# Kernel tuning notes

Measured on AMD Instinct MI355X. Metric: run time of the kernel, lower is better.

## Reference

```python
import jax, jax.numpy as jnp
import numpy as np

NUM_CAMS = 1
NUM_HEADS = 1
NUM_LEVELS = 1
NUM_POINTS = 4
NUM_DEPTH = 128
EMBED = 128  # must equal NUM_DEPTH (output_proj is applied to the depth axis)


def setup_inputs() -> dict:
    key0 = jax.random.key(0)
    ks = jax.random.split(key0, 12)
    bsv, nq, nv = 1, 1024, 1024  # nq == nv == H*W (32*32)
    off_dim = NUM_CAMS * NUM_HEADS * NUM_LEVELS * NUM_DEPTH * NUM_POINTS * 2  # 1024
    aw_dim = NUM_CAMS * NUM_HEADS * NUM_LEVELS * NUM_DEPTH * NUM_POINTS       # 512
    return {
        "query": jax.random.normal(ks[0], (bsv, nq, EMBED), jnp.float32),
        "key": jax.random.normal(ks[1], (NUM_CAMS, nv, bsv, EMBED), jnp.float32),
        "value": jax.random.normal(ks[2], (NUM_CAMS, nv, bsv, EMBED), jnp.float32),
        "ref_3d": jax.random.uniform(ks[3], (bsv * NUM_CAMS, nq * NUM_DEPTH, 2), jnp.float32),
        "spatial_shapes": jnp.array([[32, 32]], dtype=jnp.int32),
        "W_off": jax.random.normal(ks[4], (EMBED, off_dim), jnp.float32) * 0.02,
        "b_off": jax.random.normal(ks[5], (off_dim,), jnp.float32) * 0.02,
        "W_attn": jax.random.normal(ks[6], (EMBED, aw_dim), jnp.float32) * 0.02,
        "b_attn": jax.random.normal(ks[7], (aw_dim,), jnp.float32) * 0.02,
        "W_v": jax.random.normal(ks[8], (EMBED, EMBED), jnp.float32) / np.sqrt(EMBED),
        "b_v": jnp.zeros((EMBED,), jnp.float32),
        "W_o": jax.random.normal(ks[9], (EMBED, EMBED), jnp.float32) / np.sqrt(EMBED),
        "b_o": jnp.zeros((EMBED,), jnp.float32),
    }


def _bilinear_sample(val, H, W, x, y):
    """grid_sample(align_corners=False, padding=zeros) equivalent.
    val: [B, H*W, D]; x, y: [B, Q, P] in pixel coords. Returns [B, Q, P, D]."""
    B, Q, P = x.shape
    D = val.shape[-1]
    x0f = jnp.floor(x); y0f = jnp.floor(y)
    ix0 = x0f.astype(jnp.int32); iy0 = y0f.astype(jnp.int32)
    wx1 = x - x0f; wy1 = y - y0f
    wx0 = 1.0 - wx1; wy0 = 1.0 - wy1

    def corner(ix, iy, w):
        valid = (ix >= 0) & (ix < W) & (iy >= 0) & (iy < H)
        idx = jnp.clip(iy, 0, H - 1) * W + jnp.clip(ix, 0, W - 1)  # [B,Q,P]
        g = jnp.take_along_axis(val, idx.reshape(B, Q * P)[:, :, None], axis=1)
        g = g.reshape(B, Q, P, D)
        return g * (w * valid.astype(val.dtype))[..., None]

    return (corner(ix0, iy0, wx0 * wy0)
            + corner(ix0 + 1, iy0, wx1 * wy0)
            + corner(ix0, iy0 + 1, wx0 * wy1)
            + corner(ix0 + 1, iy0 + 1, wx1 * wy1))


def reference(query, key, value, ref_3d, spatial_shapes,
              W_off, b_off, W_attn, b_attn, W_v, b_v, W_o, b_o):
    bsv, nq, E = query.shape
    cams, nv, bs, _ = key.shape
    identity = query

    # key/value: [cams, nv, bs, E] -> [bsv, nv, E]
    key2 = jnp.transpose(key, (2, 0, 1, 3)).reshape(bsv, nv, E)
    val = jnp.flip(value, axis=0)
    val = jnp.transpose(val, (2, 0, 1, 3)).reshape(bsv, nv, E)
    val = val @ W_v + b_v
    val = val.reshape(bsv * cams, nv, E)  # num_heads=1 -> head_dim=E

    # offsets / attention weights (heads=levels=1 axes squeezed)
    off = (query @ W_off + b_off).reshape(bsv, nq, cams, NUM_DEPTH, NUM_POINTS, 2)
    aw = (query @ W_attn + b_attn).reshape(bsv, nq, cams, NUM_DEPTH, NUM_LEVELS * NUM_POINTS)
    aw = jax.nn.softmax(aw, axis=-1).reshape(bsv, nq, cams, NUM_DEPTH, NUM_POINTS)
    off = jnp.transpose(off, (0, 2, 1, 3, 4, 5)).reshape(bsv * cams, nq * NUM_DEPTH, NUM_POINTS, 2)
    aw = jnp.transpose(aw, (0, 2, 1, 3, 4)).reshape(bsv * cams, nq * NUM_DEPTH, NUM_POINTS)

    H = spatial_shapes[0, 0]
    W = spatial_shapes[0, 1]
    norm = jnp.stack([W, H]).astype(off.dtype)  # [W, H]
    loc = ref_3d[:, :, None, :] + off / norm    # [B, Qe, P, 2] in [0,1]
    x = loc[..., 0] * W.astype(loc.dtype) - 0.5
    y = loc[..., 1] * H.astype(loc.dtype) - 0.5

    sampled = _bilinear_sample(val, H, W, x, y)          # [B, Qe, P, E]
    out = jnp.einsum('bqpe,bqp->bqe', sampled, aw)       # weighted sum over points

    out = out.reshape(bsv, cams, nq, NUM_DEPTH, E).mean(axis=1)  # [bsv, nq, depth, E]
    out = (out * key2[:, :, None, :]).mean(axis=-1)              # [bsv, nq, depth]
    out = out @ W_o + b_o                                        # depth == EMBED
    return out + identity  # dropout = identity in eval
```

## Files before the change

kernel.cpp:

```cpp
#include <hip/hip_runtime.h>
#include <hip/hip_bf16.h>


#define NQ   1024
#define NV   1024
#define ND   128
#define NP   4
#define IMG_W 32
#define IMG_H 32

__device__ __forceinline__ void gemm_tile64(
    const float* __restrict__ A,
    const float* __restrict__ B,
    int N, bool nt,
    const float* __restrict__ bias,
    const float* __restrict__ cvec,
    float* __restrict__ C,
    int m0, int n0, float* sA, float* sB) {
  const int tid = threadIdx.x;

#pragma unroll
  for (int k = 0; k < 8; ++k) {
    int c = tid + k * 256;
    int m = c & 63, e4 = c >> 6;
    const float4 v = *(const float4*)(A + (size_t)(m0 + m) * 128 + e4 * 4);
    sA[(e4 * 4 + 0) * 64 + m] = v.x;
    sA[(e4 * 4 + 1) * 64 + m] = v.y;
    sA[(e4 * 4 + 2) * 64 + m] = v.z;
    sA[(e4 * 4 + 3) * 64 + m] = v.w;
  }
  if (nt) {
#pragma unroll
    for (int k = 0; k < 8; ++k) {
      int c = tid + k * 256;
      int n = c & 63, e4 = c >> 6;
      const float4 v = *(const float4*)(B + (size_t)(n0 + n) * 128 + e4 * 4);
      sB[(e4 * 4 + 0) * 64 + n] = v.x;
      sB[(e4 * 4 + 1) * 64 + n] = v.y;
      sB[(e4 * 4 + 2) * 64 + n] = v.z;
      sB[(e4 * 4 + 3) * 64 + n] = v.w;
    }
  } else {
#pragma unroll
    for (int k = 0; k < 8; ++k) {
      int c = tid + k * 256;
      int n4 = c & 15, e = c >> 4;
      *(float4*)(sB + e * 64 + n4 * 4) =
          *(const float4*)(B + (size_t)e * N + n0 + n4 * 4);
    }
  }
  __syncthreads();

  const int tx = tid & 15, ty = tid >> 4;
  float acc[4][4] = {};
#pragma unroll 8
  for (int e = 0; e < 128; ++e) {
    const float4 a = *(const float4*)(sA + e * 64 + ty * 4);
    const float4 b = *(const float4*)(sB + e * 64 + tx * 4);
    acc[0][0] += a.x * b.x; acc[0][1] += a.x * b.y; acc[0][2] += a.x * b.z; acc[0][3] += a.x * b.w;
    acc[1][0] += a.y * b.x; acc[1][1] += a.y * b.y; acc[1][2] += a.y * b.z; acc[1][3] += a.y * b.w;
    acc[2][0] += a.z * b.x; acc[2][1] += a.z * b.y; acc[2][2] += a.z * b.z; acc[2][3] += a.z * b.w;
    acc[3][0] += a.w * b.x; acc[3][1] += a.w * b.y; acc[3][2] += a.w * b.z; acc[3][3] += a.w * b.w;
  }

  float4 bv = make_float4(0.f, 0.f, 0.f, 0.f);
  if (bias) bv = *(const float4*)(bias + n0 + tx * 4);
#pragma unroll
  for (int i = 0; i < 4; ++i) {
    const int m = m0 + ty * 4 + i;
    float cv = cvec ? cvec[m] : 0.f;
    float4 r;
    r.x = acc[i][0] + bv.x + cv;
    r.y = acc[i][1] + bv.y + cv;
    r.z = acc[i][2] + bv.z + cv;
    r.w = acc[i][3] + bv.w + cv;
    *(float4*)(C + (size_t)m * N + n0 + tx * 4) = r;
  }
}

__global__ __launch_bounds__(256, 2) void p1_kernel(
    const float* __restrict__ query, const float* __restrict__ key,
    const float* __restrict__ W_off, const float* __restrict__ b_off,
    const float* __restrict__ W_attn, const float* __restrict__ b_attn,
    const float* __restrict__ W_v, const float* __restrict__ b_v,
    float* __restrict__ off_ws, float* __restrict__ aw_ws,
    float* __restrict__ keyp_ws, float* __restrict__ c_ws) {
  __shared__ float sA[128 * 64];
  __shared__ float sB[128 * 64];
  const int t = blockIdx.x;
  if (t < 256) {
    gemm_tile64(query, W_off, 1024, false, b_off, nullptr, off_ws,
                (t >> 4) * 64, (t & 15) * 64, sA, sB);
  } else if (t < 384) {
    const int u = t - 256;
    gemm_tile64(query, W_attn, 512, false, b_attn, nullptr, aw_ws,
                (u >> 3) * 64, (u & 7) * 64, sA, sB);
  } else if (t < 416) {
    const int u = t - 384;
    gemm_tile64(key, W_v, 128, true, nullptr, nullptr, keyp_ws,
                (u >> 1) * 64, (u & 1) * 64, sA, sB);
  } else {
    for (int i = 0; i < 4; ++i) {
      const int q = threadIdx.x + i * 256;
      float s = 0.f;
      for (int e = 0; e < 128; ++e) s += key[(size_t)q * 128 + e] * b_v[e];
      c_ws[q] = s;
    }
  }
}

__global__ __launch_bounds__(256, 2) void p2_kernel(
    const float* __restrict__ keyp_ws, const float* __restrict__ value,
    const float* __restrict__ c_ws, float* __restrict__ dotv_ws) {
  __shared__ float sA[128 * 64];
  __shared__ float sB[128 * 64];
  const int t = blockIdx.x;
  gemm_tile64(keyp_ws, value, 1024, true, nullptr, c_ws, dotv_ws,
              (t >> 4) * 64, (t & 15) * 64, sA, sB);
}

__global__ __launch_bounds__(256) void p3_kernel(
    const float* __restrict__ dotv,
    const float* __restrict__ off,
    const float* __restrict__ awr,
    const float* __restrict__ ref3d,
    const float* __restrict__ query,
    const float* __restrict__ W_o,
    const float* __restrict__ b_o,
    float* __restrict__ out) {
  __shared__ float img[2][NV];
  __shared__ float o1s[2][ND];

  const int tid = threadIdx.x;
  const int q0 = blockIdx.x * 2;

#pragma unroll
  for (int k = 0; k < 2; ++k) {
    int c = tid + k * 256;
    int qq = c >> 8, v4 = c & 255;
    *(float4*)(&img[qq][v4 * 4]) =
        *(const float4*)(dotv + (size_t)(q0 + qq) * NV + v4 * 4);
  }
  __syncthreads();

  {
    const int qq = tid >> 7;
    const int q = q0 + qq;
    const int d = tid & 127;
    const float* im = img[qq];
    const size_t qe = (size_t)q * ND + d;

    const float rx = ref3d[qe * 2 + 0];
    const float ry = ref3d[qe * 2 + 1];

    const float* awp = awr + (size_t)q * (ND * NP) + d * NP;
    const float a0 = awp[0], a1 = awp[1], a2 = awp[2], a3 = awp[3];
    const float mx = fmaxf(fmaxf(a0, a1), fmaxf(a2, a3));
    const float e0 = __expf(a0 - mx), e1 = __expf(a1 - mx),
                e2 = __expf(a2 - mx), e3 = __expf(a3 - mx);
    const float inv = 1.0f / (e0 + e1 + e2 + e3);
    const float w[4] = {e0 * inv, e1 * inv, e2 * inv, e3 * inv};

    const float* op = off + (size_t)q * (ND * NP * 2) + d * (NP * 2);

    float acc = 0.0f;
#pragma unroll
    for (int p = 0; p < NP; ++p) {
      const float x = rx * (float)IMG_W + op[p * 2 + 0] - 0.5f;
      const float y = ry * (float)IMG_H + op[p * 2 + 1] - 0.5f;
      const float xf = floorf(x), yf = floorf(y);
      const int ix0 = (int)xf, iy0 = (int)yf;
      const float wx1 = x - xf, wy1 = y - yf;
      const float wx0 = 1.0f - wx1, wy0 = 1.0f - wy1;

      float s = 0.0f;
#pragma unroll
      for (int cy = 0; cy < 2; ++cy) {
#pragma unroll
        for (int cx = 0; cx < 2; ++cx) {
          const int ix = ix0 + cx, iy = iy0 + cy;
          const bool valid = (ix >= 0) & (ix < IMG_W) & (iy >= 0) & (iy < IMG_H);
          const int cix = min(max(ix, 0), IMG_W - 1);
          const int ciy = min(max(iy, 0), IMG_H - 1);
          const float wgt = (cx ? wx1 : wx0) * (cy ? wy1 : wy0);
          s += valid ? im[ciy * IMG_W + cix] * wgt : 0.0f;
        }
      }
      acc += w[p] * s;
    }
    o1s[qq][d] = acc * (1.0f / 128.0f);
  }
  __syncthreads();

  {
    const int qq = tid >> 7;
    const int q = q0 + qq;
    const int n = tid & 127;
    float acc = b_o[n] + query[(size_t)q * 128 + n];
#pragma unroll 8
    for (int d = 0; d < 128; ++d)
      acc += o1s[qq][d] * W_o[(size_t)d * 128 + n];
    out[(size_t)q * 128 + n] = acc;
  }
}

extern "C" void kernel_launch(void* const* d_in, const int* in_sizes, int n_in,
                              void* d_out, int out_size, void* d_ws, size_t ws_size,
                              hipStream_t stream) {
  const float* query  = (const float*)d_in[0];
  const float* key    = (const float*)d_in[1];
  const float* value  = (const float*)d_in[2];
  const float* ref3d  = (const float*)d_in[3];
  const float* W_off  = (const float*)d_in[5];
  const float* b_off  = (const float*)d_in[6];
  const float* W_attn = (const float*)d_in[7];
  const float* b_attn = (const float*)d_in[8];
  const float* W_v    = (const float*)d_in[9];
  const float* b_v    = (const float*)d_in[10];
  const float* W_o    = (const float*)d_in[11];
  const float* b_o    = (const float*)d_in[12];
  float* out = (float*)d_out;

  float* ws = (float*)d_ws;
  float* off_ws  = ws;
  float* aw_ws   = off_ws + (size_t)NQ * 1024;
  float* keyp_ws = aw_ws + (size_t)NQ * 512;
  float* c_ws    = keyp_ws + (size_t)NQ * 128;
  float* dotv_ws = c_ws + 1024;

  p1_kernel<<<417, 256, 0, stream>>>(query, key, W_off, b_off, W_attn, b_attn,
                                     W_v, b_v, off_ws, aw_ws, keyp_ws, c_ws);
  p2_kernel<<<256, 256, 0, stream>>>(keyp_ws, value, c_ws, dotv_ws);
  p3_kernel<<<512, 256, 0, stream>>>(dotv_ws, off_ws, aw_ws, ref3d, query,
                                     W_o, b_o, out);
}
```

Baseline: 113.7 us.

## Fuse three kernels into one monolithic per-query-block kernel with bf16 MFMA

```diff
diff --git a/kernel.cpp b/kernel.cpp
--- a/kernel.cpp
+++ b/kernel.cpp
@@ -1,5 +1,4 @@
 #include <hip/hip_runtime.h>
-#include <hip/hip_bf16.h>
 
 
 #define NQ   1024
@@ -8,143 +7,189 @@
 #define NP   4
 #define IMG_W 32
 #define IMG_H 32
-
-__device__ __forceinline__ void gemm_tile64(
-    const float* __restrict__ A,
-    const float* __restrict__ B,
-    int N, bool nt,
-    const float* __restrict__ bias,
-    const float* __restrict__ cvec,
-    float* __restrict__ C,
-    int m0, int n0, float* sA, float* sB) {
-  const int tid = threadIdx.x;
-
-#pragma unroll
-  for (int k = 0; k < 8; ++k) {
-    int c = tid + k * 256;
-    int m = c & 63, e4 = c >> 6;
-    const float4 v = *(const float4*)(A + (size_t)(m0 + m) * 128 + e4 * 4);
-    sA[(e4 * 4 + 0) * 64 + m] = v.x;
-    sA[(e4 * 4 + 1) * 64 + m] = v.y;
-    sA[(e4 * 4 + 2) * 64 + m] = v.z;
-    sA[(e4 * 4 + 3) * 64 + m] = v.w;
-  }
-  if (nt) {
-#pragma unroll
-    for (int k = 0; k < 8; ++k) {
-      int c = tid + k * 256;
-      int n = c & 63, e4 = c >> 6;
-      const float4 v = *(const float4*)(B + (size_t)(n0 + n) * 128 + e4 * 4);
-      sB[(e4 * 4 + 0) * 64 + n] = v.x;
-      sB[(e4 * 4 + 1) * 64 + n] = v.y;
-      sB[(e4 * 4 + 2) * 64 + n] = v.z;
-      sB[(e4 * 4 + 3) * 64 + n] = v.w;
-    }
-  } else {
-#pragma unroll
-    for (int k = 0; k < 8; ++k) {
-      int c = tid + k * 256;
-      int n4 = c & 15, e = c >> 4;
-      *(float4*)(sB + e * 64 + n4 * 4) =
-          *(const float4*)(B + (size_t)e * N + n0 + n4 * 4);
-    }
-  }
-  __syncthreads();
-
-  const int tx = tid & 15, ty = tid >> 4;
-  float acc[4][4] = {};
-#pragma unroll 8
-  for (int e = 0; e < 128; ++e) {
-    const float4 a = *(const float4*)(sA + e * 64 + ty * 4);
-    const float4 b = *(const float4*)(sB + e * 64 + tx * 4);
-    acc[0][0] += a.x * b.x; acc[0][1] += a.x * b.y; acc[0][2] += a.x * b.z; acc[0][3] += a.x * b.w;
-    acc[1][0] += a.y * b.x; acc[1][1] += a.y * b.y; acc[1][2] += a.y * b.z; acc[1][3] += a.y * b.w;
-    acc[2][0] += a.z * b.x; acc[2][1] += a.z * b.y; acc[2][2] += a.z * b.z; acc[2][3] += a.z * b.w;
-    acc[3][0] += a.w * b.x; acc[3][1] += a.w * b.y; acc[3][2] += a.w * b.z; acc[3][3] += a.w * b.w;
-  }
-
-  float4 bv = make_float4(0.f, 0.f, 0.f, 0.f);
-  if (bias) bv = *(const float4*)(bias + n0 + tx * 4);
-#pragma unroll
-  for (int i = 0; i < 4; ++i) {
-    const int m = m0 + ty * 4 + i;
-    float cv = cvec ? cvec[m] : 0.f;
-    float4 r;
-    r.x = acc[i][0] + bv.x + cv;
-    r.y = acc[i][1] + bv.y + cv;
-    r.z = acc[i][2] + bv.z + cv;
-    r.w = acc[i][3] + bv.w + cv;
-    *(float4*)(C + (size_t)m * N + n0 + tx * 4) = r;
-  }
+#define QB   4
+
+typedef __attribute__((ext_vector_type(8))) short bfx8;
+typedef __attribute__((ext_vector_type(4))) float f32x4;
+
+__device__ __forceinline__ unsigned short bf_rne(float f) {
+  unsigned u = __float_as_uint(f);
+  return (unsigned short)((u + 0x7FFFu + ((u >> 16) & 1u)) >> 16);
 }
 
-__global__ __launch_bounds__(256, 2) void p1_kernel(
+__global__ __launch_bounds__(256) void mono_kernel(
     const float* __restrict__ query, const float* __restrict__ key,
+    const float* __restrict__ value, const float* __restrict__ ref3d,
     const float* __restrict__ W_off, const float* __restrict__ b_off,
     const float* __restrict__ W_attn, const float* __restrict__ b_attn,
     const float* __restrict__ W_v, const float* __restrict__ b_v,
-    float* __restrict__ off_ws, float* __restrict__ aw_ws,
-    float* __restrict__ keyp_ws, float* __restrict__ c_ws) {
-  __shared__ float sA[128 * 64];
-  __shared__ float sB[128 * 64];
-  const int t = blockIdx.x;
-  if (t < 256) {
-    gemm_tile64(query, W_off, 1024, false, b_off, nullptr, off_ws,
-                (t >> 4) * 64, (t & 15) * 64, sA, sB);
-  } else if (t < 384) {
-    const int u = t - 256;
-    gemm_tile64(query, W_attn, 512, false, b_attn, nullptr, aw_ws,
-                (u >> 3) * 64, (u & 7) * 64, sA, sB);
-  } else if (t < 416) {
-    const int u = t - 384;
-    gemm_tile64(key, W_v, 128, true, nullptr, nullptr, keyp_ws,
-                (u >> 1) * 64, (u & 1) * 64, sA, sB);
+    const float* __restrict__ W_o, const float* __restrict__ b_o,
+    float* __restrict__ out) {
+  __shared__ float q_lds[QB][128];
+  __shared__ float img[QB][NV];
+  __shared__ float off_lds[QB][1024];
+  __shared__ float aw_lds[QB][512];
+  __shared__ float c_lds[QB];
+  __shared__ __align__(16) char Ru[16384];
+  float* key_lds  = (float*)Ru;
+  float* keyp_lds = (float*)(Ru + 2048);
+  unsigned short* sval = (unsigned short*)Ru;
+  float* o1s = (float*)Ru;
+
+  const int tid = threadIdx.x;
+  const int q0 = blockIdx.x * QB;
+  const int w = tid >> 6, l = tid & 63;
+
+  if (tid < 128) {
+    ((float4*)q_lds)[tid] = ((const float4*)(query + (size_t)q0 * 128))[tid];
   } else {
-    for (int i = 0; i < 4; ++i) {
-      const int q = threadIdx.x + i * 256;
+    ((float4*)key_lds)[tid - 128] =
+        ((const float4*)(key + (size_t)q0 * 128))[tid - 128];
+  }
+  __syncthreads();
+
+  {
+    float4 aoff[QB];
+    float2 aaw[QB];
+#pragma unroll
+    for (int qq = 0; qq < QB; ++qq) {
+      aoff[qq] = make_float4(0.f, 0.f, 0.f, 0.f);
+      aaw[qq] = make_float2(0.f, 0.f);
+    }
+    const float* wo_p = W_off + (size_t)tid * 4;
+    const float* wa_p = W_attn + (size_t)tid * 2;
+#pragma unroll 4
+    for (int e4 = 0; e4 < 32; ++e4) {
+      float4 q4[QB];
+#pragma unroll
+      for (int qq = 0; qq < QB; ++qq)
+        q4[qq] = *(const float4*)(&q_lds[qq][e4 * 4]);
+#pragma unroll
+      for (int j = 0; j < 4; ++j) {
+        const int e = e4 * 4 + j;
+        const float4 w4 = *(const float4*)(wo_p + (size_t)e * 1024);
+        const float2 w2 = *(const float2*)(wa_p + (size_t)e * 512);
+#pragma unroll
+        for (int qq = 0; qq < QB; ++qq) {
+          const float* qp = (const float*)&q4[qq];
+          const float qv = qp[j];
+          aoff[qq].x = fmaf(qv, w4.x, aoff[qq].x);
+          aoff[qq].y = fmaf(qv, w4.y, aoff[qq].y);
+          aoff[qq].z = fmaf(qv, w4.z, aoff[qq].z);
+          aoff[qq].w = fmaf(qv, w4.w, aoff[qq].w);
+          aaw[qq].x = fmaf(qv, w2.x, aaw[qq].x);
+          aaw[qq].y = fmaf(qv, w2.y, aaw[qq].y);
+        }
+      }
+    }
+    const float4 bo4 = *(const float4*)(b_off + tid * 4);
+    const float2 ba2 = *(const float2*)(b_attn + tid * 2);
+#pragma unroll
+    for (int qq = 0; qq < QB; ++qq) {
+      float4 r;
+      r.x = aoff[qq].x + bo4.x; r.y = aoff[qq].y + bo4.y;
+      r.z = aoff[qq].z + bo4.z; r.w = aoff[qq].w + bo4.w;
+      *(float4*)(&off_lds[qq][tid * 4]) = r;
+      float2 r2;
+      r2.x = aaw[qq].x + ba2.x; r2.y = aaw[qq].y + ba2.y;
+      *(float2*)(&aw_lds[qq][tid * 2]) = r2;
+    }
+  }
+
+  {
+    const int h = l >> 5, e4s = l & 31;
+#pragma unroll 2
+    for (int s = 0; s < 16; ++s) {
+      const int i = w * 32 + s * 2 + h;
+      const float4 wv = *(const float4*)(W_v + (size_t)i * 128 + e4s * 4);
+      float p[QB];
+#pragma unroll
+      for (int qq = 0; qq < QB; ++qq) {
+        const float4 k4 = *(const float4*)(key_lds + qq * 128 + e4s * 4);
+        p[qq] = fmaf(wv.x, k4.x,
+                fmaf(wv.y, k4.y, fmaf(wv.z, k4.z, wv.w * k4.w)));
+      }
+#pragma unroll
+      for (int m = 1; m < 32; m <<= 1)
+#pragma unroll
+        for (int qq = 0; qq < QB; ++qq) p[qq] += __shfl_xor(p[qq], m);
+      if (e4s == 0)
+#pragma unroll
+        for (int qq = 0; qq < QB; ++qq) keyp_lds[qq * 128 + i] = p[qq];
+    }
+    if (tid < QB) {
       float s = 0.f;
-      for (int e = 0; e < 128; ++e) s += key[(size_t)q * 128 + e] * b_v[e];
-      c_ws[q] = s;
-    }
-  }
-}
-
-__global__ __launch_bounds__(256, 2) void p2_kernel(
-    const float* __restrict__ keyp_ws, const float* __restrict__ value,
-    const float* __restrict__ c_ws, float* __restrict__ dotv_ws) {
-  __shared__ float sA[128 * 64];
-  __shared__ float sB[128 * 64];
-  const int t = blockIdx.x;
-  gemm_tile64(keyp_ws, value, 1024, true, nullptr, c_ws, dotv_ws,
-              (t >> 4) * 64, (t & 15) * 64, sA, sB);
-}
-
-__global__ __launch_bounds__(256) void p3_kernel(
-    const float* __restrict__ dotv,
-    const float* __restrict__ off,
-    const float* __restrict__ awr,
-    const float* __restrict__ ref3d,
-    const float* __restrict__ query,
-    const float* __restrict__ W_o,
-    const float* __restrict__ b_o,
-    float* __restrict__ out) {
-  __shared__ float img[2][NV];
-  __shared__ float o1s[2][ND];
-
-  const int tid = threadIdx.x;
-  const int q0 = blockIdx.x * 2;
-
-#pragma unroll
-  for (int k = 0; k < 2; ++k) {
-    int c = tid + k * 256;
-    int qq = c >> 8, v4 = c & 255;
-    *(float4*)(&img[qq][v4 * 4]) =
-        *(const float4*)(dotv + (size_t)(q0 + qq) * NV + v4 * 4);
-  }
-  __syncthreads();
-
-  {
-    const int qq = tid >> 7;
+      for (int e = 0; e < 128; e += 4) {
+        const float4 bv = *(const float4*)(b_v + e);
+        const float4 k4 = *(const float4*)(key_lds + tid * 128 + e);
+        s = fmaf(bv.x, k4.x,
+            fmaf(bv.y, k4.y, fmaf(bv.z, k4.z, fmaf(bv.w, k4.w, s))));
+      }
+      c_lds[tid] = s;
+    }
+  }
+  __syncthreads();
+
+  bfx8 afrag[4];
+  {
+    const int row = l & 15, g = l >> 4;
+#pragma unroll
+    for (int ks = 0; ks < 4; ++ks) {
+      bfx8 a;
+      if (row < QB) {
+        const float* kp = keyp_lds + row * 128 + ks * 32 + g * 8;
+#pragma unroll
+        for (int j = 0; j < 8; ++j) a[j] = (short)bf_rne(kp[j]);
+      } else {
+#pragma unroll
+        for (int j = 0; j < 8; ++j) a[j] = 0;
+      }
+      afrag[ks] = a;
+    }
+  }
+  __syncthreads();
+
+  for (int vt = 0; vt < 16; ++vt) {
+#pragma unroll
+    for (int it = 0; it < 4; ++it) {
+      const int c = tid + it * 256;
+      const int r = c >> 4, cc = c & 15;
+      const float* p = value + (size_t)(vt * 64 + r) * 128 + cc * 8;
+      const float4 f0 = *(const float4*)p;
+      const float4 f1 = *(const float4*)(p + 4);
+      bfx8 vv;
+      vv[0] = (short)bf_rne(f0.x); vv[1] = (short)bf_rne(f0.y);
+      vv[2] = (short)bf_rne(f0.z); vv[3] = (short)bf_rne(f0.w);
+      vv[4] = (short)bf_rne(f1.x); vv[5] = (short)bf_rne(f1.y);
+      vv[6] = (short)bf_rne(f1.z); vv[7] = (short)bf_rne(f1.w);
+      const int byte = r * 256 + ((cc * 16) ^ ((r & 15) << 4));
+      *(bfx8*)((char*)sval + byte) = vv;
+    }
+    __syncthreads();
+
+    {
+      const int col = l & 15, g = l >> 4;
+      const int r = w * 16 + col;
+      f32x4 acc = {0.f, 0.f, 0.f, 0.f};
+#pragma unroll
+      for (int ks = 0; ks < 4; ++ks) {
+        const int colb = (ks * 64 + g * 16) ^ (col << 4);
+        const bfx8 bfr = *(const bfx8*)((const char*)sval + r * 256 + colb);
+        acc = __builtin_amdgcn_mfma_f32_16x16x32_bf16(afrag[ks], bfr, acc,
+                                                      0, 0, 0);
+      }
+      if (g == 0) {
+        const int v = vt * 64 + w * 16 + col;
+#pragma unroll
+        for (int i = 0; i < QB; ++i) img[i][v] = acc[i] + c_lds[i];
+      }
+    }
+    __syncthreads();
+  }
+
+#pragma unroll
+  for (int pass = 0; pass < 2; ++pass) {
+    const int qq = (tid >> 7) + 2 * pass;
     const int q = q0 + qq;
     const int d = tid & 127;
     const float* im = img[qq];
@@ -153,15 +198,15 @@
     const float rx = ref3d[qe * 2 + 0];
     const float ry = ref3d[qe * 2 + 1];
 
-    const float* awp = awr + (size_t)q * (ND * NP) + d * NP;
+    const float* awp = &aw_lds[qq][d * NP];
     const float a0 = awp[0], a1 = awp[1], a2 = awp[2], a3 = awp[3];
     const float mx = fmaxf(fmaxf(a0, a1), fmaxf(a2, a3));
     const float e0 = __expf(a0 - mx), e1 = __expf(a1 - mx),
                 e2 = __expf(a2 - mx), e3 = __expf(a3 - mx);
     const float inv = 1.0f / (e0 + e1 + e2 + e3);
-    const float w[4] = {e0 * inv, e1 * inv, e2 * inv, e3 * inv};
-
-    const float* op = off + (size_t)q * (ND * NP * 2) + d * (NP * 2);
+    const float wgt4[4] = {e0 * inv, e1 * inv, e2 * inv, e3 * inv};
+
+    const float* op = &off_lds[qq][d * (NP * 2)];
 
     float acc = 0.0f;
 #pragma unroll
@@ -186,21 +231,25 @@
           s += valid ? im[ciy * IMG_W + cix] * wgt : 0.0f;
         }
       }
-      acc += w[p] * s;
-    }
-    o1s[qq][d] = acc * (1.0f / 128.0f);
-  }
-  __syncthreads();
-
-  {
-    const int qq = tid >> 7;
-    const int q = q0 + qq;
+      acc += wgt4[p] * s;
+    }
+    o1s[qq * ND + d] = acc * (1.0f / 128.0f);
+  }
+  __syncthreads();
+
+  {
+    const int qqA = tid >> 7, qqB = qqA + 2;
     const int n = tid & 127;
-    float acc = b_o[n] + query[(size_t)q * 128 + n];
+    float acc0 = b_o[n] + q_lds[qqA][n];
+    float acc1 = b_o[n] + q_lds[qqB][n];
 #pragma unroll 8
-    for (int d = 0; d < 128; ++d)
-      acc += o1s[qq][d] * W_o[(size_t)d * 128 + n];
-    out[(size_t)q * 128 + n] = acc;
+    for (int d = 0; d < 128; ++d) {
+      const float wv = W_o[(size_t)d * 128 + n];
+      acc0 = fmaf(o1s[qqA * ND + d], wv, acc0);
+      acc1 = fmaf(o1s[qqB * ND + d], wv, acc1);
+    }
+    out[(size_t)(q0 + qqA) * 128 + n] = acc0;
+    out[(size_t)(q0 + qqB) * 128 + n] = acc1;
   }
 }
 
@@ -221,16 +270,7 @@
   const float* b_o    = (const float*)d_in[12];
   float* out = (float*)d_out;
 
-  float* ws = (float*)d_ws;
-  float* off_ws  = ws;
-  float* aw_ws   = off_ws + (size_t)NQ * 1024;
-  float* keyp_ws = aw_ws + (size_t)NQ * 512;
-  float* c_ws    = keyp_ws + (size_t)NQ * 128;
-  float* dotv_ws = c_ws + 1024;
-
-  p1_kernel<<<417, 256, 0, stream>>>(query, key, W_off, b_off, W_attn, b_attn,
-                                     W_v, b_v, off_ws, aw_ws, keyp_ws, c_ws);
-  p2_kernel<<<256, 256, 0, stream>>>(keyp_ws, value, c_ws, dotv_ws);
-  p3_kernel<<<512, 256, 0, stream>>>(dotv_ws, off_ws, aw_ws, ref3d, query,
-                                     W_o, b_o, out);
+  mono_kernel<<<NQ / QB, 256, 0, stream>>>(query, key, value, ref3d,
+                                           W_off, b_off, W_attn, b_attn,
+                                           W_v, b_v, W_o, b_o, out);
 }
```

Measured after the change: 119.4 us. +5.0%, slower.
